# Performance work log

Measured on AMD Instinct MI355X. Metric: run time of the kernel, lower is better.

The kernel has to match this reference:

```python
import jax, jax.numpy as jnp
import numpy as np

B, L, V, E, H, NH = 64, 256, 30000, 300, 200, 4
ENC = 2 * H
DH = ENC // NH
SCALING = 1000.0   # 1 / test_temperature (eval path of the module)
BUDGET_PCT = 20.0  # self.budget


def setup_inputs() -> dict:
    key = jax.random.key(0)
    ks = jax.random.split(key, 16)
    x = jax.random.randint(ks[0], (B, L), 0, V)
    lengths = jax.random.randint(ks[1], (B,), L // 2, L + 1)
    mask = jnp.arange(L)[None, :] < lengths[:, None]
    z = jax.random.normal(ks[2], (B, L), jnp.float32)
    g = lambda k, sh, sc: jax.random.normal(k, sh, jnp.float32) * sc
    embed_W = g(ks[3], (V, E), 0.1)
    Wi_f = g(ks[4], (E, 4 * H), 0.05); Wh_f = g(ks[5], (H, 4 * H), 0.05); b_f = jnp.zeros((4 * H,), jnp.float32)
    Wi_b = g(ks[6], (E, 4 * H), 0.05); Wh_b = g(ks[7], (H, 4 * H), 0.05); b_b = jnp.zeros((4 * H,), jnp.float32)
    Wk = g(ks[8], (ENC, ENC), 0.05)
    Wv = g(ks[9], (ENC, ENC), 0.05)
    q = g(ks[10], (NH, DH), 0.1)          # learned pooling state pattern per head
    Wo = g(ks[11], (ENC, ENC), 0.05)       # Hopfield output projection
    out_W = g(ks[12], (ENC, 1), 0.05)
    out_b = jnp.zeros((1,), jnp.float32)
    return dict(x=x, z=z, mask=mask, embed_W=embed_W, Wi_f=Wi_f, Wh_f=Wh_f, b_f=b_f,
                Wi_b=Wi_b, Wh_b=Wh_b, b_b=b_b, Wk=Wk, Wv=Wv, q=q, Wo=Wo,
                out_W=out_W, out_b=out_b)


def _lstm_dir(xproj, mask, Wh, reverse):
    # xproj: [B,L,4H] (x @ Wi + b precomputed), torch gate order i,f,g,o
    def step(carry, inp):
        h, c = carry
        xt, mt = inp
        gates = xt + h @ Wh
        i, f, gg, o = jnp.split(gates, 4, axis=-1)
        c_new = jax.nn.sigmoid(f) * c + jax.nn.sigmoid(i) * jnp.tanh(gg)
        h_new = jax.nn.sigmoid(o) * jnp.tanh(c_new)
        mt = mt[:, None]
        h = jnp.where(mt, h_new, h)  # packed-sequence semantics: freeze past length
        c = jnp.where(mt, c_new, c)
        return (h, c), h
    h0 = jnp.zeros((xproj.shape[0], Wh.shape[0]), xproj.dtype)
    _, hs = jax.lax.scan(step, (h0, h0), (xproj.transpose(1, 0, 2), mask.T), reverse=reverse)
    return hs.transpose(1, 0, 2)  # [B,L,H]


def _budget_project(scores, mask, budget):
    # SparseMAP for budget factor (transition=0): project scores onto
    # {p in [0,1]^L : sum p <= budget}, per (sample, head). scores: [B,NH,L]
    NEG = jnp.float32(-1e9)
    s = jnp.where(mask[:, None, :], scores, NEG)
    b = budget[:, None]  # [B,1]
    p0 = jnp.clip(s, 0.0, 1.0)
    need = jnp.sum(p0, -1) > b
    s_sg = jax.lax.stop_gradient(s)

    def body(i, lohi):
        lo, hi = lohi
        mid = 0.5 * (lo + hi)
        val = jnp.sum(jnp.clip(s_sg - mid[..., None], 0.0, 1.0), -1)
        gt = val > b
        return jnp.where(gt, mid, lo), jnp.where(gt, hi, mid)

    lo = jnp.zeros(s.shape[:2], s.dtype)
    hi = jnp.max(jnp.where(mask[:, None, :], s_sg, 0.0), -1) + 1.0
    lo, hi = jax.lax.fori_loop(0, 60, body, (lo, hi))
    tau0 = 0.5 * (lo + hi)
    # differentiable closed-form tau from the active set (implicit grad of projection)
    r = s - tau0[..., None]
    free = (r > 0.0) & (r < 1.0) & mask[:, None, :]
    hi1 = (r >= 1.0) & mask[:, None, :]
    n_free = jnp.sum(free, -1)
    tau = (jnp.sum(jnp.where(free, s, 0.0), -1) + jnp.sum(hi1, -1) - b) / jnp.maximum(n_free, 1)
    tau = jnp.where(n_free > 0, tau, tau0)
    p = jnp.clip(s - tau[..., None], 0.0, 1.0)
    return jnp.where(need[..., None], p, p0)


def reference(x, z, mask, embed_W, Wi_f, Wh_f, b_f, Wi_b, Wh_b, b_b, Wk, Wv, q, Wo, out_W, out_b):
    emb = embed_W[x]  # [B,L,E]; dropout is identity in eval
    hf = _lstm_dir(emb @ Wi_f + b_f, mask, Wh_f, reverse=False)
    hb = _lstm_dir(emb @ Wi_b + b_b, mask, Wh_b, reverse=True)
    h1 = jnp.concatenate([hf, hb], axis=-1)  # [B,L,ENC]
    K = (h1 @ Wk).reshape(B, L, NH, DH)
    Vv = (h1 @ Wv).reshape(B, L, NH, DH)
    scores = SCALING * jnp.einsum('hd,blhd->bhl', q, K)  # [B,NH,L]
    lengths = jnp.sum(mask, -1)
    budget = jnp.round(BUDGET_PCT / 100.0 * lengths).astype(jnp.float32)
    p = _budget_project(scores, mask, budget)  # [B,NH,L] sparse, sum<=budget
    pooled = jnp.einsum('bhl,blhd->bhd', p, Vv).reshape(B, ENC) @ Wo  # [B,ENC]
    y = jax.nn.sigmoid(pooled @ out_W + out_b)  # [B,1]
    zp = jnp.where(mask, jnp.mean(p, axis=1), 0.0)  # [B,L] rationale probs
    return y, zp
```

## Files before the change

kernel.cpp:

```cpp
#include <hip/hip_runtime.h>
#include <math.h>

#define B_      64
#define L_      256
#define V_      30000
#define E_      300
#define H_      200
#define G4_     800
#define ENC_    400
#define NH_     4
#define DH_     100
#define SCALING_ 1000.0f

__device__ __forceinline__ float sigmoidf_(float x) { return 1.0f / (1.0f + expf(-x)); }

__device__ __forceinline__ float blockSum256(float v, float* red) {
    for (int off = 32; off > 0; off >>= 1) v += __shfl_down(v, off);
    __syncthreads();
    if ((threadIdx.x & 63) == 0) red[threadIdx.x >> 6] = v;
    __syncthreads();
    return red[0] + red[1] + red[2] + red[3];
}
__device__ __forceinline__ float blockMax256(float v, float* red) {
    for (int off = 32; off > 0; off >>= 1) v = fmaxf(v, __shfl_down(v, off));
    __syncthreads();
    if ((threadIdx.x & 63) == 0) red[threadIdx.x >> 6] = v;
    __syncthreads();
    return fmaxf(fmaxf(red[0], red[1]), fmaxf(red[2], red[3]));
}

#define GTM 128
#define GTN 64
#define GKC 16
#define SA_LD (GTM + 4)
#define SB_LD (GTN + 4)
#define FR_GEMM  3200
#define FR_PREP  (FR_GEMM + 64)
#define FR_WEFF  (FR_PREP + 13)
#define FR_PACK  (FR_WEFF + 1250)
__global__ __launch_bounds__(256) void k_front(const int* __restrict__ x,
        const float* __restrict__ embW,
        const float* __restrict__ Wi_f, const float* __restrict__ b_f,
        const float* __restrict__ Wi_b, const float* __restrict__ b_b,
        float* __restrict__ xproj,
        const void* __restrict__ maskraw, int* __restrict__ lengths,
        float* __restrict__ budget,
        const float* __restrict__ Wk, const float* __restrict__ Wv,
        const float* __restrict__ q, const float* __restrict__ Wo,
        const float* __restrict__ outW, float* __restrict__ Weff,
        const float* __restrict__ Wh_f, const float* __restrict__ Wh_b,
        float* __restrict__ Wp) {
    __shared__ float sA[GKC * SA_LD];
    __shared__ float sB[GKC * SB_LD];
    __shared__ int srow[GTM];
    __shared__ float sOW[ENC_];
    __shared__ float sW2[ENC_];
    __shared__ float red[4];
    int tid = threadIdx.x;
    int blk = blockIdx.x;

    if (blk < FR_GEMM) {
        int tm0 = (blk & 127) * GTM;
        int tn0 = (blk >> 7) * GTN;
        if (tid < GTM) srow[tid] = x[tm0 + tid];
        __syncthreads();
        int tx = tid & 15, ty = tid >> 4;
        float acc[8][4];
#pragma unroll
        for (int u = 0; u < 8; u++)
#pragma unroll
            for (int v = 0; v < 4; v++) acc[u][v] = 0.0f;

        int mm = tid >> 1, kk8 = (tid & 1) * 8;
        int kkB = tid >> 4, c4 = (tid & 15) * 4;
        int colB = tn0 + c4;
        const float* bbase = (colB < G4_) ? (Wi_f + colB) : (Wi_b + (colB - G4_));

        for (int k0 = 0; k0 < E_; k0 += GKC) {
            const float* arow = embW + (size_t)srow[mm] * E_ + k0 + kk8;
            if (k0 + GKC <= E_) {
                float4 a0 = *(const float4*)(arow);
                float4 a1 = *(const float4*)(arow + 4);
                sA[(kk8 + 0) * SA_LD + mm] = a0.x;
                sA[(kk8 + 1) * SA_LD + mm] = a0.y;
                sA[(kk8 + 2) * SA_LD + mm] = a0.z;
                sA[(kk8 + 3) * SA_LD + mm] = a0.w;
                sA[(kk8 + 4) * SA_LD + mm] = a1.x;
                sA[(kk8 + 5) * SA_LD + mm] = a1.y;
                sA[(kk8 + 6) * SA_LD + mm] = a1.z;
                sA[(kk8 + 7) * SA_LD + mm] = a1.w;
            } else {
#pragma unroll
                for (int i = 0; i < 8; i++) {
                    int k = k0 + kk8 + i;
                    sA[(kk8 + i) * SA_LD + mm] = (k < E_) ? arow[i] : 0.0f;
                }
            }
            {
                int kB = k0 + kkB;
                float4 bv = make_float4(0.f, 0.f, 0.f, 0.f);
                if (kB < E_) bv = *(const float4*)(bbase + (size_t)kB * G4_);
                *(float4*)&sB[kkB * SB_LD + c4] = bv;
            }
            __syncthreads();
#pragma unroll
            for (int kk2 = 0; kk2 < GKC; kk2++) {
                float4 a0 = *(const float4*)&sA[kk2 * SA_LD + ty * 8];
                float4 a1 = *(const float4*)&sA[kk2 * SA_LD + ty * 8 + 4];
                float4 b0 = *(const float4*)&sB[kk2 * SB_LD + tx * 4];
                float av[8] = {a0.x, a0.y, a0.z, a0.w, a1.x, a1.y, a1.z, a1.w};
                float bv[4] = {b0.x, b0.y, b0.z, b0.w};
#pragma unroll
                for (int u = 0; u < 8; u++)
#pragma unroll
                    for (int v = 0; v < 4; v++) acc[u][v] = fmaf(av[u], bv[v], acc[u][v]);
            }
            __syncthreads();
        }
        int col = tn0 + tx * 4;
        float4 bias = (col < G4_) ? *(const float4*)(b_f + col)
                                  : *(const float4*)(b_b + (col - G4_));
#pragma unroll
        for (int u = 0; u < 8; u++) {
            int m = tm0 + ty * 8 + u;
            float4 o;
            o.x = acc[u][0] + bias.x;
            o.y = acc[u][1] + bias.y;
            o.z = acc[u][2] + bias.z;
            o.w = acc[u][3] + bias.w;
            *(float4*)&xproj[(size_t)m * 1600 + col] = o;
        }
    } else if (blk < FR_PREP) {
        int b = blk - FR_GEMM;
        const unsigned char* mb = (const unsigned char*)maskraw;
        bool is_byte = (mb[1] != 0);
        const int* mi = (const int*)maskraw;
        int v = is_byte ? (int)mb[b * L_ + tid] : mi[b * L_ + tid];
        float cnt = blockSum256((v != 0) ? 1.0f : 0.0f, red);
        if (tid == 0) {
            int c = (int)(cnt + 0.5f);
            lengths[b] = c;
            budget[b] = rintf(0.2f * (float)c);
        }
    } else if (blk < FR_WEFF) {
        for (int i = tid; i < ENC_; i += 256) sOW[i] = outW[i];
        __syncthreads();
        for (int e2 = tid; e2 < ENC_; e2 += 256) {
            float s = 0.0f;
            for (int j2 = 0; j2 < ENC_; j2++)
                s = fmaf(Wo[(size_t)e2 * ENC_ + j2], sOW[j2], s);
            sW2[e2] = s;
        }
        __syncthreads();
        int idx = (blk - FR_PREP) * 256 + tid;
        if (idx < ENC_ * 8) {
            int e = idx >> 3, c = idx & 7;
            int h = c & 3;
            bool isV = (c >= 4);
            const float* M = isV ? Wv : Wk;
            float s = 0.0f;
            for (int d = 0; d < DH_; d++) {
                float wq = isV ? sW2[h * DH_ + d] : q[h * DH_ + d];
                s = fmaf(M[(size_t)e * ENC_ + h * DH_ + d], wq, s);
            }
            Weff[idx] = s;
        }
    } else {
        int idx = (blk - FR_WEFF) * 256 + tid;
        if (idx < 2 * H_ * H_ * 4) {
            int dir = idx / (H_ * H_ * 4);
            int r = idx % (H_ * H_ * 4);
            int k = r / (H_ * 4);
            int r2 = r % (H_ * 4);
            int j = r2 >> 2, g = r2 & 3;
            const float* Wh = dir ? Wh_b : Wh_f;
            Wp[idx] = Wh[(size_t)k * G4_ + g * H_ + j];
        }
    }
}

#define KS2 50
__global__ __launch_bounds__(512, 2) void k_lstm(const float* __restrict__ xproj,
        const float4* __restrict__ Wp, const int* __restrict__ lengths,
        float* __restrict__ hf, float* __restrict__ hb,
        unsigned long long* __restrict__ hxS) {
    int pid = blockIdx.x;
    int chain = pid & 127;
    int half = pid >> 7;
    int partner = pid ^ 128;
    int b = chain >> 1, dir = chain & 1;
    int jbase = half * 100;
    const float4* W = Wp + (size_t)dir * H_ * H_;
    float* hout = dir ? hb : hf;
    int len = lengths[b];
    __shared__ float sh[256];
    __shared__ float4 sPart[4][128];
    __shared__ int scnt;
    int tid = threadIdx.x;
    int q = tid >> 7, j = tid & 127;
    bool act = (j < 100);
    int u = jbase + j;
    bool partnerQ = ((q >> 1) == (half ^ 1));
    int pq0 = (half ^ 1) * 2;

    float4 w[KS2];
    if (act) {
        const float4* wp = W + (size_t)(q * KS2) * H_ + u;
#pragma unroll
        for (int k = 0; k < KS2; k++) w[k] = wp[(size_t)k * H_];
    }
    if (tid < H_) sh[tid] = 0.0f;
    if (tid == 0) scnt = 0;
    float c = 0.0f;
    float hv_prev = 0.0f;
    int t_prev = -1;
    __syncthreads();
    const float* xp = xproj + (size_t)b * L_ * 1600 + dir * G4_;
    const float4* h4 = (const float4*)(sh + q * KS2);
    const float2* h2t = (const float2*)(sh + q * KS2 + 48);

    for (int s = 0; s < len; s++) {
        int t = dir ? (len - 1 - s) : s;
        if (tid < 100 && t_prev >= 0)
            hout[((size_t)b * L_ + t_prev) * H_ + jbase + tid] = hv_prev;
        if (s > 0 && q == pq0 && j < 100) {
            size_t idx = ((size_t)(((s - 1) & 1) * 256 + partner)) * 128 + j;
            unsigned long long got;
            do {
                got = __hip_atomic_load(&hxS[idx], __ATOMIC_RELAXED,
                                        __HIP_MEMORY_SCOPE_AGENT);
            } while ((unsigned)(got >> 32) != (unsigned)s);
            sh[(half ^ 1) * 100 + j] = __uint_as_float((unsigned)got);
            __threadfence_block();
            __hip_atomic_fetch_add(&scnt, 1, __ATOMIC_RELAXED,
                                   __HIP_MEMORY_SCOPE_WORKGROUP);
        }
        if (act) {
            if (partnerQ && s > 0) {
                int target = 100 * s;
                while (__hip_atomic_load(&scnt, __ATOMIC_RELAXED,
                                         __HIP_MEMORY_SCOPE_WORKGROUP) < target) {}
            }
            float xv = xp[(size_t)t * 1600 + q * H_ + u];
            float4 acc = make_float4(0.f, 0.f, 0.f, 0.f);
#pragma unroll
            for (int k4 = 0; k4 < 12; k4++) {
                float4 hk = h4[k4];
                const float4 w0 = w[k4 * 4 + 0], w1 = w[k4 * 4 + 1];
                const float4 w2 = w[k4 * 4 + 2], w3 = w[k4 * 4 + 3];
                acc.x = fmaf(hk.x, w0.x, acc.x); acc.y = fmaf(hk.x, w0.y, acc.y);
                acc.z = fmaf(hk.x, w0.z, acc.z); acc.w = fmaf(hk.x, w0.w, acc.w);
                acc.x = fmaf(hk.y, w1.x, acc.x); acc.y = fmaf(hk.y, w1.y, acc.y);
                acc.z = fmaf(hk.y, w1.z, acc.z); acc.w = fmaf(hk.y, w1.w, acc.w);
                acc.x = fmaf(hk.z, w2.x, acc.x); acc.y = fmaf(hk.z, w2.y, acc.y);
                acc.z = fmaf(hk.z, w2.z, acc.z); acc.w = fmaf(hk.z, w2.w, acc.w);
                acc.x = fmaf(hk.w, w3.x, acc.x); acc.y = fmaf(hk.w, w3.y, acc.y);
                acc.z = fmaf(hk.w, w3.z, acc.z); acc.w = fmaf(hk.w, w3.w, acc.w);
            }
            {
                float2 ht = *h2t;
                const float4 w0 = w[48], w1 = w[49];
                acc.x = fmaf(ht.x, w0.x, acc.x); acc.y = fmaf(ht.x, w0.y, acc.y);
                acc.z = fmaf(ht.x, w0.z, acc.z); acc.w = fmaf(ht.x, w0.w, acc.w);
                acc.x = fmaf(ht.y, w1.x, acc.x); acc.y = fmaf(ht.y, w1.y, acc.y);
                acc.z = fmaf(ht.y, w1.z, acc.z); acc.w = fmaf(ht.y, w1.w, acc.w);
            }
            if (q == 0) acc.x += xv;
            else if (q == 1) acc.y += xv;
            else if (q == 2) acc.z += xv;
            else acc.w += xv;
            sPart[q][j] = acc;
        }
        __syncthreads();
        if (tid < 100) {
            float4 p0 = sPart[0][tid], p1 = sPart[1][tid];
            float4 p2 = sPart[2][tid], p3 = sPart[3][tid];
            float ai = p0.x + p1.x + p2.x + p3.x;
            float af = p0.y + p1.y + p2.y + p3.y;
            float ag = p0.z + p1.z + p2.z + p3.z;
            float ao = p0.w + p1.w + p2.w + p3.w;
            float ii = sigmoidf_(ai), ff = sigmoidf_(af);
            float gg = tanhf(ag), oo = sigmoidf_(ao);
            c = ff * c + ii * gg;
            float hv = oo * tanhf(c);
            sh[jbase + tid] = hv;
            unsigned long long pk = ((unsigned long long)(unsigned)(s + 1) << 32)
                                  | (unsigned long long)__float_as_uint(hv);
            __hip_atomic_store(&hxS[((size_t)((s & 1) * 256 + pid)) * 128 + tid], pk,
                               __ATOMIC_RELAXED, __HIP_MEMORY_SCOPE_AGENT);
            hv_prev = hv; t_prev = t;
        }
        __syncthreads();
    }
    if (tid < 100 && t_prev >= 0)
        hout[((size_t)b * L_ + t_prev) * H_ + jbase + tid] = hv_prev;
    for (int i = tid; i < (L_ - len) * 100; i += 512) {
        int t = len + i / 100, uu = jbase + i % 100;
        hout[((size_t)b * L_ + t) * H_ + uu] = dir ? 0.0f : sh[uu];
    }
}

__global__ __launch_bounds__(256) void k_proj(const float* __restrict__ hf,
        const float* __restrict__ hb, const float* __restrict__ Weff,
        float* __restrict__ scores, float* __restrict__ vproj) {
    __shared__ float sW[ENC_ * 8];
    int tid = threadIdx.x;
    for (int i = tid; i < ENC_ * 8; i += 256) sW[i] = Weff[i];
    __syncthreads();
    int pos = blockIdx.x * 32 + (tid >> 3);
    int o = tid & 7;
    int b = pos >> 8, l = pos & 255;
    const float* hfr = hf + (size_t)pos * H_;
    const float* hbr = hb + (size_t)pos * H_;
    float s = 0.0f;
#pragma unroll 4
    for (int e = 0; e < H_; e++) s = fmaf(hfr[e], sW[e * 8 + o], s);
#pragma unroll 4
    for (int e = 0; e < H_; e++) s = fmaf(hbr[e], sW[(H_ + e) * 8 + o], s);
    if (o < NH_) scores[((size_t)b * NH_ + o) * L_ + l] = SCALING_ * s;
    else        vproj[(size_t)pos * NH_ + (o - NH_)] = s;
}

__global__ __launch_bounds__(256) void k_budget(const float* __restrict__ scores,
        const int* __restrict__ lengths, const float* __restrict__ budget,
        float* __restrict__ p) {
    __shared__ float red[4];
    int bh = blockIdx.x;
    int b = bh >> 2;
    int l = threadIdx.x;
    int len = lengths[b];
    float bud = budget[b];
    bool m = (l < len);
    float s = m ? scores[(size_t)bh * L_ + l] : -1.0e9f;
    float p0 = fminf(fmaxf(s, 0.0f), 1.0f);
    float sum_p0 = blockSum256(p0, red);
    bool need = (sum_p0 > bud);
    float hi = blockMax256(m ? s : 0.0f, red) + 1.0f;
    float lo = 0.0f;
    for (int it = 0; it < 60; it++) {
        float mid = 0.5f * (lo + hi);
        float val = blockSum256(fminf(fmaxf(s - mid, 0.0f), 1.0f), red);
        if (val > bud) lo = mid; else hi = mid;
    }
    float tau0 = 0.5f * (lo + hi);
    float r = s - tau0;
    bool fr  = (r > 0.0f) && (r < 1.0f) && m;
    bool h1f = (r >= 1.0f) && m;
    float n_free   = blockSum256(fr ? 1.0f : 0.0f, red);
    float sum_free = blockSum256(fr ? s : 0.0f, red);
    float n_hi     = blockSum256(h1f ? 1.0f : 0.0f, red);
    float tau = (sum_free + n_hi - bud) / fmaxf(n_free, 1.0f);
    tau = (n_free > 0.0f) ? tau : tau0;
    float pv = fminf(fmaxf(s - tau, 0.0f), 1.0f);
    p[(size_t)bh * L_ + l] = need ? pv : p0;
}

__global__ __launch_bounds__(256) void k_final(const float* __restrict__ p,
        const float* __restrict__ vproj, const int* __restrict__ lengths,
        const float* __restrict__ out_b, float* __restrict__ dout) {
    __shared__ float red[4];
    int b = blockIdx.x;
    int l = threadIdx.x;
    int len = lengths[b];
    float p0 = p[((size_t)b * NH_ + 0) * L_ + l];
    float p1 = p[((size_t)b * NH_ + 1) * L_ + l];
    float p2 = p[((size_t)b * NH_ + 2) * L_ + l];
    float p3 = p[((size_t)b * NH_ + 3) * L_ + l];
    dout[B_ + (size_t)b * L_ + l] = (l < len) ? 0.25f * (p0 + p1 + p2 + p3) : 0.0f;
    const float* vp = vproj + ((size_t)b * L_ + l) * NH_;
    float contrib = p0 * vp[0] + p1 * vp[1] + p2 * vp[2] + p3 * vp[3];
    float tot = blockSum256(contrib, red);
    if (l == 0) dout[b] = 1.0f / (1.0f + expf(-(tot + out_b[0])));
}

extern "C" void kernel_launch(void* const* d_in, const int* in_sizes, int n_in,
                              void* d_out, int out_size, void* d_ws, size_t ws_size,
                              hipStream_t stream) {
    const int*   x    = (const int*)d_in[0];
    const void*  mask = d_in[2];
    const float* embW = (const float*)d_in[3];
    const float* Wi_f = (const float*)d_in[4];
    const float* Wh_f = (const float*)d_in[5];
    const float* b_f  = (const float*)d_in[6];
    const float* Wi_b = (const float*)d_in[7];
    const float* Wh_b = (const float*)d_in[8];
    const float* b_b  = (const float*)d_in[9];
    const float* Wk   = (const float*)d_in[10];
    const float* Wv   = (const float*)d_in[11];
    const float* q    = (const float*)d_in[12];
    const float* Wo   = (const float*)d_in[13];
    const float* outW = (const float*)d_in[14];
    const float* outb = (const float*)d_in[15];
    float* dout = (float*)d_out;

    float* ws     = (float*)d_ws;
    float* xproj  = ws;
    float* hf     = xproj + (size_t)16384 * 1600;
    float* hb     = hf + (size_t)16384 * 200;
    float* scores = hb + (size_t)16384 * 200;
    float* vproj  = scores + 65536;
    float* p      = vproj + 65536;
    float* Weff   = p + 65536;
    float* w2     = Weff + 3200;
    float* budget = w2 + 400;
    int*   lengths= (int*)(budget + 64);
    float* Wp     = (float*)(lengths + 64);

    unsigned long long* hxS = (unsigned long long*)scores;

    k_front<<<FR_PACK, 256, 0, stream>>>(x, embW, Wi_f, b_f, Wi_b, b_b, xproj,
                                         mask, lengths, budget,
                                         Wk, Wv, q, Wo, outW, Weff,
                                         Wh_f, Wh_b, Wp);

    {
        const float4* Wp4 = (const float4*)Wp;
        void* args[] = { (void*)&xproj, (void*)&Wp4, (void*)&lengths,
                         (void*)&hf, (void*)&hb, (void*)&hxS };
        hipLaunchCooperativeKernel((const void*)k_lstm, dim3(256), dim3(512),
                                   args, 0, stream);
    }

    k_proj<<<(B_ * L_) / 32, 256, 0, stream>>>(hf, hb, Weff, scores, vproj);
    k_budget<<<B_ * NH_, 256, 0, stream>>>(scores, lengths, budget, p);
    k_final<<<B_, 256, 0, stream>>>(p, vproj, lengths, outb, dout);
}
```

Measured before the change: 866.8 us.

## Widen embedding GEMM tile to 128 columns and fuse budget projection with final pooling

The embedding-projection GEMM tile widens from 128x64 to 128x128 with an 8x8 per-thread accumulator. This halves the number of GEMM blocks and increases register-level reuse, with guards for the padded last column tile. The budget projection and final pooling kernels merge into one 1024-thread block per sample, where each group of 256 threads handles one head. This removes one launch and the global round trip of p, but the 64 large blocks now do the 60-iteration bisection with more barriers per reduction.

```diff
diff --git a/kernel.cpp b/kernel.cpp
--- a/kernel.cpp
+++ b/kernel.cpp
@@ -21,24 +21,17 @@
     __syncthreads();
     return red[0] + red[1] + red[2] + red[3];
 }
-__device__ __forceinline__ float blockMax256(float v, float* red) {
-    for (int off = 32; off > 0; off >>= 1) v = fmaxf(v, __shfl_down(v, off));
-    __syncthreads();
-    if ((threadIdx.x & 63) == 0) red[threadIdx.x >> 6] = v;
-    __syncthreads();
-    return fmaxf(fmaxf(red[0], red[1]), fmaxf(red[2], red[3]));
-}
 
 #define GTM 128
-#define GTN 64
+#define GTN 128
 #define GKC 16
 #define SA_LD (GTM + 4)
-#define SB_LD (GTN + 4)
-#define FR_GEMM  3200
+#define SB_LD (GTN + 8)
+#define FR_GEMM  1664
 #define FR_PREP  (FR_GEMM + 64)
 #define FR_WEFF  (FR_PREP + 13)
 #define FR_PACK  (FR_WEFF + 1250)
-__global__ __launch_bounds__(256) void k_front(const int* __restrict__ x,
+__global__ __launch_bounds__(256, 2) void k_front(const int* __restrict__ x,
         const float* __restrict__ embW,
         const float* __restrict__ Wi_f, const float* __restrict__ b_f,
         const float* __restrict__ Wi_b, const float* __restrict__ b_b,
@@ -60,21 +53,25 @@
     int blk = blockIdx.x;
 
     if (blk < FR_GEMM) {
-        int tm0 = (blk & 127) * GTM;
-        int tn0 = (blk >> 7) * GTN;
+        int rowb = blk & 127, colb = blk >> 7;
+        int tm0 = rowb * GTM;
+        int tn0 = colb * GTN;
         if (tid < GTM) srow[tid] = x[tm0 + tid];
         __syncthreads();
         int tx = tid & 15, ty = tid >> 4;
-        float acc[8][4];
+        float acc[8][8];
 #pragma unroll
         for (int u = 0; u < 8; u++)
 #pragma unroll
-            for (int v = 0; v < 4; v++) acc[u][v] = 0.0f;
+            for (int v = 0; v < 8; v++) acc[u][v] = 0.0f;
 
         int mm = tid >> 1, kk8 = (tid & 1) * 8;
-        int kkB = tid >> 4, c4 = (tid & 15) * 4;
-        int colB = tn0 + c4;
-        const float* bbase = (colB < G4_) ? (Wi_f + colB) : (Wi_b + (colB - G4_));
+        int kkB = tid >> 4, c8 = (tid & 15) * 8;
+        int colB = tn0 + c8;
+        bool bok = (colB < 2 * G4_);
+        const float* bbase = bok ? ((colB < G4_) ? (Wi_f + colB)
+                                                 : (Wi_b + (colB - G4_)))
+                                 : Wi_f;
 
         for (int k0 = 0; k0 < E_; k0 += GKC) {
             const float* arow = embW + (size_t)srow[mm] * E_ + k0 + kk8;
@@ -98,37 +95,53 @@
             }
             {
                 int kB = k0 + kkB;
-                float4 bv = make_float4(0.f, 0.f, 0.f, 0.f);
-                if (kB < E_) bv = *(const float4*)(bbase + (size_t)kB * G4_);
-                *(float4*)&sB[kkB * SB_LD + c4] = bv;
+                float4 bv0 = make_float4(0.f, 0.f, 0.f, 0.f);
+                float4 bv1 = make_float4(0.f, 0.f, 0.f, 0.f);
+                if (bok && kB < E_) {
+                    bv0 = *(const float4*)(bbase + (size_t)kB * G4_);
+                    bv1 = *(const float4*)(bbase + (size_t)kB * G4_ + 4);
+                }
+                *(float4*)&sB[kkB * SB_LD + c8] = bv0;
+                *(float4*)&sB[kkB * SB_LD + c8 + 4] = bv1;
             }
             __syncthreads();
 #pragma unroll
             for (int kk2 = 0; kk2 < GKC; kk2++) {
                 float4 a0 = *(const float4*)&sA[kk2 * SA_LD + ty * 8];
                 float4 a1 = *(const float4*)&sA[kk2 * SA_LD + ty * 8 + 4];
-                float4 b0 = *(const float4*)&sB[kk2 * SB_LD + tx * 4];
+                float4 b0 = *(const float4*)&sB[kk2 * SB_LD + tx * 8];
+                float4 b1 = *(const float4*)&sB[kk2 * SB_LD + tx * 8 + 4];
                 float av[8] = {a0.x, a0.y, a0.z, a0.w, a1.x, a1.y, a1.z, a1.w};
-                float bv[4] = {b0.x, b0.y, b0.z, b0.w};
+                float bv[8] = {b0.x, b0.y, b0.z, b0.w, b1.x, b1.y, b1.z, b1.w};
 #pragma unroll
                 for (int u = 0; u < 8; u++)
 #pragma unroll
-                    for (int v = 0; v < 4; v++) acc[u][v] = fmaf(av[u], bv[v], acc[u][v]);
+                    for (int v = 0; v < 8; v++)
+                        acc[u][v] = fmaf(av[u], bv[v], acc[u][v]);
             }
             __syncthreads();
         }
-        int col = tn0 + tx * 4;
-        float4 bias = (col < G4_) ? *(const float4*)(b_f + col)
-                                  : *(const float4*)(b_b + (col - G4_));
-#pragma unroll
-        for (int u = 0; u < 8; u++) {
-            int m = tm0 + ty * 8 + u;
-            float4 o;
-            o.x = acc[u][0] + bias.x;
-            o.y = acc[u][1] + bias.y;
-            o.z = acc[u][2] + bias.z;
-            o.w = acc[u][3] + bias.w;
-            *(float4*)&xproj[(size_t)m * 1600 + col] = o;
+        int col = tn0 + tx * 8;
+        if (col < 2 * G4_) {
+            float4 bias0, bias1;
+            if (col < G4_) {
+                bias0 = *(const float4*)(b_f + col);
+                bias1 = *(const float4*)(b_f + col + 4);
+            } else {
+                bias0 = *(const float4*)(b_b + (col - G4_));
+                bias1 = *(const float4*)(b_b + (col - G4_) + 4);
+            }
+#pragma unroll
+            for (int u = 0; u < 8; u++) {
+                int m = tm0 + ty * 8 + u;
+                float4 o0, o1;
+                o0.x = acc[u][0] + bias0.x; o0.y = acc[u][1] + bias0.y;
+                o0.z = acc[u][2] + bias0.z; o0.w = acc[u][3] + bias0.w;
+                o1.x = acc[u][4] + bias1.x; o1.y = acc[u][5] + bias1.y;
+                o1.z = acc[u][6] + bias1.z; o1.w = acc[u][7] + bias1.w;
+                *(float4*)&xproj[(size_t)m * 1600 + col] = o0;
+                *(float4*)&xproj[(size_t)m * 1600 + col + 4] = o1;
+            }
         }
     } else if (blk < FR_PREP) {
         int b = blk - FR_GEMM;
@@ -321,56 +334,84 @@
     else        vproj[(size_t)pos * NH_ + (o - NH_)] = s;
 }
 
-__global__ __launch_bounds__(256) void k_budget(const float* __restrict__ scores,
+__global__ __launch_bounds__(1024) void k_bf(const float* __restrict__ scores,
         const int* __restrict__ lengths, const float* __restrict__ budget,
-        float* __restrict__ p) {
-    __shared__ float red[4];
-    int bh = blockIdx.x;
-    int b = bh >> 2;
-    int l = threadIdx.x;
+        const float* __restrict__ vproj, const float* __restrict__ out_b,
+        float* __restrict__ dout) {
+    __shared__ float sp[4][256];
+    __shared__ float red[16];
+    int b = blockIdx.x;
+    int tid = threadIdx.x;
+    int g = tid >> 8, l = tid & 255;
     int len = lengths[b];
     float bud = budget[b];
     bool m = (l < len);
-    float s = m ? scores[(size_t)bh * L_ + l] : -1.0e9f;
+    float s = m ? scores[((size_t)(b * NH_ + g)) * L_ + l] : -1.0e9f;
+
+#define GSUM(OUTV, INV)                                                        \
+    {                                                                          \
+        float _v = (INV);                                                      \
+        for (int off = 32; off > 0; off >>= 1) _v += __shfl_down(_v, off);     \
+        __syncthreads();                                                       \
+        if ((tid & 63) == 0) red[tid >> 6] = _v;                               \
+        __syncthreads();                                                       \
+        OUTV = red[g * 4] + red[g * 4 + 1] + red[g * 4 + 2] + red[g * 4 + 3];  \
+        __syncthreads();                                                       \
+    }
+#define GMAX(OUTV, INV)                                                        \
+    {                                                                          \
+        float _v = (INV);                                                      \
+        for (int off = 32; off > 0; off >>= 1) _v = fmaxf(_v, __shfl_down(_v, off)); \
+        __syncthreads();                                                       \
+        if ((tid & 63) == 0) red[tid >> 6] = _v;                               \
+        __syncthreads();                                                       \
+        OUTV = fmaxf(fmaxf(red[g * 4], red[g * 4 + 1]),                        \
+                     fmaxf(red[g * 4 + 2], red[g * 4 + 3]));                   \
+        __syncthreads();                                                       \
+    }
+
     float p0 = fminf(fmaxf(s, 0.0f), 1.0f);
-    float sum_p0 = blockSum256(p0, red);
+    float sum_p0; GSUM(sum_p0, p0);
     bool need = (sum_p0 > bud);
-    float hi = blockMax256(m ? s : 0.0f, red) + 1.0f;
+    float hi; GMAX(hi, m ? s : 0.0f);
+    hi += 1.0f;
     float lo = 0.0f;
     for (int it = 0; it < 60; it++) {
         float mid = 0.5f * (lo + hi);
-        float val = blockSum256(fminf(fmaxf(s - mid, 0.0f), 1.0f), red);
+        float val; GSUM(val, fminf(fmaxf(s - mid, 0.0f), 1.0f));
         if (val > bud) lo = mid; else hi = mid;
     }
     float tau0 = 0.5f * (lo + hi);
     float r = s - tau0;
     bool fr  = (r > 0.0f) && (r < 1.0f) && m;
     bool h1f = (r >= 1.0f) && m;
-    float n_free   = blockSum256(fr ? 1.0f : 0.0f, red);
-    float sum_free = blockSum256(fr ? s : 0.0f, red);
-    float n_hi     = blockSum256(h1f ? 1.0f : 0.0f, red);
+    float n_free;   GSUM(n_free,   fr ? 1.0f : 0.0f);
+    float sum_free; GSUM(sum_free, fr ? s : 0.0f);
+    float n_hi;     GSUM(n_hi,     h1f ? 1.0f : 0.0f);
     float tau = (sum_free + n_hi - bud) / fmaxf(n_free, 1.0f);
     tau = (n_free > 0.0f) ? tau : tau0;
     float pv = fminf(fmaxf(s - tau, 0.0f), 1.0f);
-    p[(size_t)bh * L_ + l] = need ? pv : p0;
-}
-
-__global__ __launch_bounds__(256) void k_final(const float* __restrict__ p,
-        const float* __restrict__ vproj, const int* __restrict__ lengths,
-        const float* __restrict__ out_b, float* __restrict__ dout) {
-    __shared__ float red[4];
-    int b = blockIdx.x;
-    int l = threadIdx.x;
-    int len = lengths[b];
-    float p0 = p[((size_t)b * NH_ + 0) * L_ + l];
-    float p1 = p[((size_t)b * NH_ + 1) * L_ + l];
-    float p2 = p[((size_t)b * NH_ + 2) * L_ + l];
-    float p3 = p[((size_t)b * NH_ + 3) * L_ + l];
-    dout[B_ + (size_t)b * L_ + l] = (l < len) ? 0.25f * (p0 + p1 + p2 + p3) : 0.0f;
-    const float* vp = vproj + ((size_t)b * L_ + l) * NH_;
-    float contrib = p0 * vp[0] + p1 * vp[1] + p2 * vp[2] + p3 * vp[3];
-    float tot = blockSum256(contrib, red);
-    if (l == 0) dout[b] = 1.0f / (1.0f + expf(-(tot + out_b[0])));
+    sp[g][l] = need ? pv : p0;
+    __syncthreads();
+
+    float contrib = 0.0f;
+    if (g == 0) {
+        float P0 = sp[0][l], P1 = sp[1][l], P2 = sp[2][l], P3 = sp[3][l];
+        const float* vp = vproj + ((size_t)b * L_ + l) * NH_;
+        contrib = P0 * vp[0] + P1 * vp[1] + P2 * vp[2] + P3 * vp[3];
+        dout[B_ + (size_t)b * L_ + l] = m ? 0.25f * (P0 + P1 + P2 + P3) : 0.0f;
+    }
+    for (int off = 32; off > 0; off >>= 1) contrib += __shfl_down(contrib, off);
+    __syncthreads();
+    if ((tid & 63) == 0) red[tid >> 6] = contrib;
+    __syncthreads();
+    if (tid == 0) {
+        float tot = 0.0f;
+        for (int i = 0; i < 16; i++) tot += red[i];
+        dout[b] = 1.0f / (1.0f + expf(-(tot + out_b[0])));
+    }
+#undef GSUM
+#undef GMAX
 }
 
 extern "C" void kernel_launch(void* const* d_in, const int* in_sizes, int n_in,
@@ -422,6 +463,5 @@
     }
 
     k_proj<<<(B_ * L_) / 32, 256, 0, stream>>>(hf, hb, Weff, scores, vproj);
-    k_budget<<<B_ * NH_, 256, 0, stream>>>(scores, lengths, budget, p);
-    k_final<<<B_, 256, 0, stream>>>(p, vproj, lengths, outb, dout);
-}
+    k_bf<<<B_, 1024, 0, stream>>>(scores, lengths, budget, vproj, outb, dout);
+}
```

Result: no change. 870.6 us (+0.4%).
